# Kernel optimization log

Measured on AMD Instinct MI355X. Metric: run time of the kernel, lower is better.

Reference implementation:

```python
import jax, jax.numpy as jnp
import numpy as np

K = 20          # neighbors, hardcoded in module
SLOPE = 0.2     # LeakyReLU negative slope
EPS = 1e-5      # BatchNorm eps (eval mode, running_mean=0, running_var=1)


def _knn_idx(x, k):
    # x: (B, N, C) -> (B, N, k) indices of k nearest neighbors (includes self)
    xx = jnp.sum(x * x, axis=-1)                      # (B, N)
    inner = jnp.einsum('bnc,bmc->bnm', x, x)          # (B, N, N)
    neg_sqdist = 2.0 * inner - xx[:, :, None] - xx[:, None, :]
    _, idx = jax.lax.top_k(neg_sqdist, k)
    return idx


def _graph_feature(x, k):
    # x: (B, N, C) -> edge features (B, N, k, 2C) = [x_j - x_i, x_i]
    idx = _knn_idx(x, k)
    feat = jax.vmap(lambda xt, ix: xt[ix])(x, idx)    # (B, N, k, C)
    xc = jnp.broadcast_to(x[:, :, None, :], feat.shape)
    return jnp.concatenate([feat - xc, xc], axis=-1)


def _bn_lrelu(h, g, b):
    # eval-mode BN (mean=0, var=1) + LeakyReLU(0.2)
    h = h * (g / jnp.sqrt(1.0 + EPS)) + b
    return jnp.where(h >= 0, h, SLOPE * h)


def _edge_conv(x, W, g, b):
    # EdgeConv block: graph feature -> 1x1 conv -> BN -> LeakyReLU -> max over k
    e = _graph_feature(x, K)                          # (B, N, k, 2C)
    h = jnp.einsum('bnkc,oc->bnko', e, W)
    h = _bn_lrelu(h, g, b)
    return jnp.max(h, axis=2)                         # (B, N, O)


def reference(x, W1, g1, b1, W2, g2, b2, W3, g3, b3, W4, g4, b4, W5, g5, b5, Wemb):
    # x: (B, N, 3) point cloud
    x1 = _edge_conv(x, W1, g1, b1)    # (B, N, 64)
    x2 = _edge_conv(x1, W2, g2, b2)   # (B, N, 64)
    x3 = _edge_conv(x2, W3, g3, b3)   # (B, N, 128)
    x4 = _edge_conv(x3, W4, g4, b4)   # (B, N, 256)
    h = jnp.concatenate([x1, x2, x3, x4], axis=-1)    # (B, N, 512)
    h = jnp.einsum('bnc,oc->bno', h, W5)              # conv5 (1x1)
    h = _bn_lrelu(h, g5, b5)
    h = jnp.max(h, axis=1)                            # global max pool -> (B, 512)
    feat = h[:, None, :]                              # (B, 1, 512)
    embedding = h @ Wemb.T                            # (B, 256)
    return (feat, embedding)


def setup_inputs() -> dict:
    key = jax.random.key(0)
    ks = jax.random.split(key, 18)
    B, N = 8, 2048
    num_features = 256

    def w(k, o, i):
        return jax.random.normal(k, (o, i), dtype=jnp.float32) * (1.0 / np.sqrt(i))

    return {
        'x':  jax.random.normal(ks[0], (B, N, 3), dtype=jnp.float32),
        'W1': w(ks[1], 64, 6),
        'g1': jnp.ones((64,), jnp.float32),  'b1': jnp.zeros((64,), jnp.float32),
        'W2': w(ks[2], 64, 128),
        'g2': jnp.ones((64,), jnp.float32),  'b2': jnp.zeros((64,), jnp.float32),
        'W3': w(ks[3], 128, 128),
        'g3': jnp.ones((128,), jnp.float32), 'b3': jnp.zeros((128,), jnp.float32),
        'W4': w(ks[4], 256, 256),
        'g4': jnp.ones((256,), jnp.float32), 'b4': jnp.zeros((256,), jnp.float32),
        'W5': w(ks[5], 512, 512),
        'g5': jnp.ones((512,), jnp.float32), 'b5': jnp.zeros((512,), jnp.float32),
        'Wemb': w(ks[6], num_features, 512),
    }
```

## Files before the change

### kernel.cpp

```cpp
#include <hip/hip_runtime.h>
#include <hip/hip_bf16.h>

#define BB 8
#define NN 2048
#define KK 20
#define BN (BB*NN)
#define RSQ 0.99999500003749969f

constexpr size_t OFF_XX  = 0;
constexpr size_t OFF_X1  = OFF_XX  + BN;
constexpr size_t OFF_X2  = OFF_X1  + (size_t)BN*64;
constexpr size_t OFF_X3  = OFF_X2  + (size_t)BN*64;
constexpr size_t OFF_X4  = OFF_X3  + (size_t)BN*128;
constexpr size_t OFF_SC  = OFF_X4  + (size_t)BN*256;
constexpr size_t OFF_ID  = OFF_SC  + (size_t)BN*160;
constexpr size_t OFF_W5T = OFF_ID  + (size_t)BN*20;
constexpr size_t OFF_MX  = OFF_W5T + 512*512;
constexpr size_t OFF_MN  = OFF_MX  + BB*512;
constexpr size_t OFF_WT2 = OFF_MN  + BB*512;
constexpr size_t OFF_WT3 = OFF_WT2 + 8192;
constexpr size_t OFF_WT4 = OFF_WT3 + 16384;
constexpr size_t WS_END  = OFF_WT4 + 65536;
constexpr size_t OFF_BIG = WS_END;
constexpr size_t OFF_XCAT = OFF_BIG + (size_t)16*1024*1024;
constexpr size_t WS_BIG_END = OFF_BIG + (size_t)BB*NN*NN;
static_assert(OFF_ID - OFF_X3 >= (size_t)4096*2048, "fallback dual dist fits");
static_assert(OFF_XCAT + (size_t)BN*768 <= WS_BIG_END, "xcat h/m/l fits in dist region");

typedef unsigned short u16;
typedef __attribute__((ext_vector_type(8))) short short8;
typedef __attribute__((ext_vector_type(8))) unsigned short ushort8;
typedef __attribute__((ext_vector_type(4))) float f32x4;

constexpr size_t WTS_2H = 0,      WTS_2M = 8192,   WTS_2L = 16384;
constexpr size_t WTS_3H = 24576,  WTS_3M = 40960,  WTS_3L = 57344;
constexpr size_t WTS_4H = 73728,  WTS_4M = 139264, WTS_4L = 204800;

__device__ inline unsigned encf(float f){ unsigned u=__float_as_uint(f); return (u&0x80000000u)? ~u : (u|0x80000000u); }
__device__ inline float decf(unsigned e){ unsigned u=(e&0x80000000u)? (e&0x7fffffffu) : ~e; return __uint_as_float(u); }
__device__ inline float lrelu(float h){ return h>=0.f ? h : 0.2f*h; }
__device__ inline u16 bf16rne(float x){
  unsigned u = __float_as_uint(x);
  return (u16)((u + 0x7FFFu + ((u>>16)&1u)) >> 16);
}
__device__ inline float bf16f(u16 h){ return __uint_as_float((unsigned)h<<16); }
__device__ inline void bf16split3(float v, u16& h, u16& m, u16& l){
  h = bf16rne(v);  float r1 = v  - bf16f(h);
  m = bf16rne(r1); float r2 = r1 - bf16f(m);
  l = bf16rne(r2);
}

__device__ inline float readlane_f(float v, int sl){
  return __int_as_float(__builtin_amdgcn_readlane(__float_as_int(v), sl));
}

#define INSERT_CAND(cv, ci) { \
  unsigned long long mge = __ballot((lv > cv) || (lv == cv && li < ci)); \
  int pos = __popcll(mge); \
  float upv = __shfl_up(lv, 1); \
  int   upi = __shfl_up(li, 1); \
  bool shift = (lane > pos) && (lane < KK); \
  lv = (lane == pos) ? cv : (shift ? upv : lv); \
  li = (lane == pos) ? ci : (shift ? upi : li); \
  theta = readlane_f(lv, KK-1); }

#define BITONIC64_DESC(v, vi) { \
  _Pragma("unroll") \
  for(int k=2; k<=64; k<<=1){ \
    _Pragma("unroll") \
    for(int j=k>>1; j>=1; j>>=1){ \
      float ov = __shfl_xor(v, j); \
      int   oi = __shfl_xor(vi, j); \
      int partner = lane ^ j; \
      bool keepFirst = (((lane & k) == 0)) == (lane < partner); \
      bool before = (v > ov) || (v == ov && vi < oi); \
      if(keepFirst != before){ v = ov; vi = oi; } \
    } \
  } }


__global__ void prep_k(const float* W5, const float* W2, const float* W3, const float* W4,
                       float* W5T, float* WT2, float* WT3, float* WT4,
                       u16* w5h, u16* w5m, u16* w5l, u16* wts,
                       unsigned* mx, unsigned* mn, int big){
  int i = blockIdx.x*256 + threadIdx.x;
  if(!big){ int o = i>>9, c = i&511; W5T[c*512+o] = W5[i]; }
  {
    int rg = i>>13, kt = (i>>9)&15, l = (i>>3)&63, j = i&7;
    int o = rg*16 + (l&15);
    int c = kt*32 + ((l>>4)<<3) + j;
    u16 h,m,lo; bf16split3(W5[(size_t)o*512 + c], h, m, lo);
    w5h[i]=h; w5m[i]=m; w5l[i]=lo; }
  if(i < 65536){ int c = i>>9, o = i&511;
    WT4[i] = (o<256) ? W4[(size_t)o*256 + c] : W4[(size_t)(o-256)*256 + 128 + c]; }
  if(i < 16384){ int c = i>>8, o = i&255;
    WT3[i] = (o<128) ? W3[(size_t)o*128 + c] : W3[(size_t)(o-128)*128 + 64 + c]; }
  if(i <  8192){ int c = i>>7, o = i&127;
    WT2[i] = (o<64) ? W2[(size_t)o*128 + c] : W2[(size_t)(o-64)*128 + 64 + c]; }
  if(big){
    if(i < 65536){
      int rg=i>>11, kt=(i>>9)&3, l=(i>>3)&63, j=i&7;
      int o = rg*16 + (l&15);
      int c = kt*32 + ((l>>4)<<3) + j;
      float v = (o<256) ? W4[(size_t)o*256 + c] : W4[(size_t)(o-256)*256 + 128 + c];
      u16 h,m,lo; bf16split3(v,h,m,lo);
      wts[WTS_4H+i]=h; wts[WTS_4M+i]=m; wts[WTS_4L+i]=lo; }
  }
  if(i <  4096){ mx[i] = 0x007FFFFFu; mn[i] = 0xFF800000u; }
}

template<int C>
__launch_bounds__(256) __global__ void sqnorm_k(const float* X, float* xx){
  int i = blockIdx.x*256 + threadIdx.x;
  const float* r = X + (size_t)i*C;
  float s = 0.f;
  #pragma unroll
  for(int c=0;c<C;c++) s = fmaf(r[c], r[c], s);
  xx[i] = s;
}

template<int C>
__launch_bounds__(256) __global__ void split_k(const float* __restrict__ X,
    u16* __restrict__ xh, u16* __restrict__ xm, u16* __restrict__ xl){
  constexpr int KT = C/32;
  const size_t t = (size_t)blockIdx.x*256 + threadIdx.x;
  const int l = (int)(t & 63);
  const size_t tile = t >> 6;
  const int kt = (int)(tile & (KT-1));
  const size_t rgG = tile / KT;
  const size_t row = rgG*16 + (l & 15);
  const int k = kt*32 + ((l>>4)<<3);
  const float* p = X + row*C + k;
  float4 v0 = *(const float4*)p;
  float4 v1 = *(const float4*)(p+4);
  float vs[8] = {v0.x,v0.y,v0.z,v0.w,v1.x,v1.y,v1.z,v1.w};
  ushort8 H,M,L;
  #pragma unroll
  for(int j=0;j<8;j++){ u16 h,m,lo; bf16split3(vs[j],h,m,lo); H[j]=h; M[j]=m; L[j]=lo; }
  *(ushort8*)(xh + t*8) = H;
  *(ushort8*)(xm + t*8) = M;
  *(ushort8*)(xl + t*8) = L;
}

#define FMA_ROW(I) \
  acc[I][0]=fmaf(a,b0v,acc[I][0]); acc[I][1]=fmaf(a,b1v,acc[I][1]); \
  acc[I][2]=fmaf(a,b2v,acc[I][2]); acc[I][3]=fmaf(a,b3v,acc[I][3]); \
  acc[I][4]=fmaf(a,b4v,acc[I][4]); acc[I][5]=fmaf(a,b5v,acc[I][5]); \
  acc[I][6]=fmaf(a,b6v,acc[I][6]); acc[I][7]=fmaf(a,b7v,acc[I][7]);

template<int C>
__launch_bounds__(256) __global__ void gemm_dist_k(const float* __restrict__ X, const float* __restrict__ xx,
                                                   float* __restrict__ dist, int b0){
  constexpr int AST = 188;
  __shared__ __align__(16) float a_sh[16*AST];
  __shared__ __align__(16) float b_sh[16*AST];
  __shared__ float sxn[128], sxm[128];
  const int tid = threadIdx.x;
  const int b   = b0 + blockIdx.z;
  const int mtile = blockIdx.x*128;
  const int ntile = blockIdx.y*128;
  const int tn = tid & 15, tm = tid >> 4;
  const float* Xb  = X  + (size_t)b*NN*C;
  const float* xxb = xx + (size_t)b*NN;
  if(tid < 128) sxn[tid] = xxb[ntile + tid];
  else          sxm[tid-128] = xxb[mtile + tid-128];
  float acc[8][8];
  #pragma unroll
  for(int i=0;i<8;i++){
    #pragma unroll
    for(int j=0;j<8;j++) acc[i][j]=0.f;
  }
  for(int cc=0; cc<C; cc+=16){
    __syncthreads();
    #pragma unroll
    for(int s=0;s<2;s++){
      int ii = tid + 256*s; int r = ii>>2, q = ii&3;
      int pr = r + 4*(r>>3);
      float4 va = *(const float4*)&Xb[(size_t)(ntile + r)*C + cc + 4*q];
      a_sh[(4*q+0)*AST + pr]=va.x; a_sh[(4*q+1)*AST + pr]=va.y;
      a_sh[(4*q+2)*AST + pr]=va.z; a_sh[(4*q+3)*AST + pr]=va.w;
      float4 vb = *(const float4*)&Xb[(size_t)(mtile + r)*C + cc + 4*q];
      b_sh[(4*q+0)*AST + pr]=vb.x; b_sh[(4*q+1)*AST + pr]=vb.y;
      b_sh[(4*q+2)*AST + pr]=vb.z; b_sh[(4*q+3)*AST + pr]=vb.w;
    }
    __syncthreads();
    #pragma unroll
    for(int c=0;c<16;c++){
      float4 A0 = *(const float4*)&a_sh[c*AST + 12*tn];
      float4 A1 = *(const float4*)&a_sh[c*AST + 12*tn + 4];
      float4 B0 = *(const float4*)&b_sh[c*AST + 12*tm];
      float4 B1 = *(const float4*)&b_sh[c*AST + 12*tm + 4];
      float b0v=B0.x,b1v=B0.y,b2v=B0.z,b3v=B0.w,b4v=B1.x,b5v=B1.y,b6v=B1.z,b7v=B1.w;
      float a;
      a=A0.x; FMA_ROW(0)
      a=A0.y; FMA_ROW(1)
      a=A0.z; FMA_ROW(2)
      a=A0.w; FMA_ROW(3)
      a=A1.x; FMA_ROW(4)
      a=A1.y; FMA_ROW(5)
      a=A1.z; FMA_ROW(6)
      a=A1.w; FMA_ROW(7)
    }
  }
  float xnr[8], xmr[8];
  #pragma unroll
  for(int i=0;i<8;i++){ xnr[i]=sxn[tn*8+i]; xmr[i]=sxm[tm*8+i]; }
  const size_t rowb = (size_t)blockIdx.z*NN + ntile + tn*8;
  #pragma unroll
  for(int i=0;i<8;i++){
    float4 w0, w1;
    w0.x=(2.f*acc[i][0]-xnr[i])-xmr[0]; w0.y=(2.f*acc[i][1]-xnr[i])-xmr[1];
    w0.z=(2.f*acc[i][2]-xnr[i])-xmr[2]; w0.w=(2.f*acc[i][3]-xnr[i])-xmr[3];
    w1.x=(2.f*acc[i][4]-xnr[i])-xmr[4]; w1.y=(2.f*acc[i][5]-xnr[i])-xmr[5];
    w1.z=(2.f*acc[i][6]-xnr[i])-xmr[6]; w1.w=(2.f*acc[i][7]-xnr[i])-xmr[7];
    float* dp = dist + (rowb + i)*NN + mtile + tm*8;
    *(float4*)dp = w0;
    *(float4*)(dp+4) = w1;
  }
}

template<int C>
__launch_bounds__(256) __global__ void mfma_dist_k(const u16* __restrict__ xh, const u16* __restrict__ xm,
    const u16* __restrict__ xl, const float* __restrict__ xx, float* __restrict__ dist, int b0){
  constexpr int KT = C/32;
  const int tid = threadIdx.x;
  const int l  = tid & 63, wv = tid >> 6;
  const int lg = l >> 4, lr = l & 15;
  const int cz = blockIdx.z;
  const int b  = b0 + cz;
  const int qrow0 = blockIdx.y*128 + (wv>>1)*64;
  const int crow0 = blockIdx.x*128 + (wv&1)*64;
  const size_t brg = (size_t)b*(NN/16);
  f32x4 acc[4][4];
  #pragma unroll
  for(int m=0;m<4;m++){
    #pragma unroll
    for(int n=0;n<4;n++) acc[m][n] = (f32x4){0.f,0.f,0.f,0.f};
  }
  const size_t abase = (brg + (qrow0>>4))*KT*512 + (size_t)l*8;
  const size_t bbase = (brg + (crow0>>4))*KT*512 + (size_t)l*8;
  for(int kt=0; kt<KT; kt++){
    short8 Ah[4], Am[4], Al[4], Bh[4], Bm[4], Bl[4];
    #pragma unroll
    for(int m=0;m<4;m++){
      size_t o = abase + (size_t)(m*KT + kt)*512;
      Ah[m] = *(const short8*)(xh + o);
      Am[m] = *(const short8*)(xm + o);
      Al[m] = *(const short8*)(xl + o);
    }
    #pragma unroll
    for(int n=0;n<4;n++){
      size_t o = bbase + (size_t)(n*KT + kt)*512;
      Bh[n] = *(const short8*)(xh + o);
      Bm[n] = *(const short8*)(xm + o);
      Bl[n] = *(const short8*)(xl + o);
    }
    #pragma unroll
    for(int m=0;m<4;m++){
      #pragma unroll
      for(int n=0;n<4;n++){
        acc[m][n] = __builtin_amdgcn_mfma_f32_16x16x32_bf16(Ah[m], Bh[n], acc[m][n], 0, 0, 0);
        acc[m][n] = __builtin_amdgcn_mfma_f32_16x16x32_bf16(Ah[m], Bm[n], acc[m][n], 0, 0, 0);
        acc[m][n] = __builtin_amdgcn_mfma_f32_16x16x32_bf16(Am[m], Bh[n], acc[m][n], 0, 0, 0);
        acc[m][n] = __builtin_amdgcn_mfma_f32_16x16x32_bf16(Ah[m], Bl[n], acc[m][n], 0, 0, 0);
        acc[m][n] = __builtin_amdgcn_mfma_f32_16x16x32_bf16(Al[m], Bh[n], acc[m][n], 0, 0, 0);
        acc[m][n] = __builtin_amdgcn_mfma_f32_16x16x32_bf16(Am[m], Bm[n], acc[m][n], 0, 0, 0);
      }
    }
  }
  const float* xxb = xx + (size_t)b*NN;
  float xxc[4];
  #pragma unroll
  for(int n=0;n<4;n++) xxc[n] = xxb[crow0 + n*16 + lr];
  #pragma unroll
  for(int m=0;m<4;m++){
    #pragma unroll
    for(int r=0;r<4;r++){
      int qr = qrow0 + m*16 + 4*lg + r;
      float xq = xxb[qr];
      float* dp = dist + ((size_t)cz*NN + qr)*NN + crow0;
      #pragma unroll
      for(int n=0;n<4;n++) dp[n*16 + lr] = (2.f*acc[m][n][r] - xq) - xxc[n];
    }
  }
}

__launch_bounds__(256) __global__ void sel_k(const float* __restrict__ dist, int* __restrict__ id,
                                             int b0, int nrows){
  const int w = (blockIdx.x*256 + threadIdx.x) >> 6;
  const int lane = threadIdx.x & 63;
  if(w >= nrows) return;
  const float* dr = dist + (size_t)w*NN;
  float4 c0 = *(const float4*)&dr[4*lane];
  float cd0[4] = {c0.x, c0.y, c0.z, c0.w};
  int jbest = 0; float v = cd0[0];
  #pragma unroll
  for(int j=1;j<4;j++){ if(cd0[j] > v){ v = cd0[j]; jbest = j; } }
  int vi = 4*lane + jbest;
  BITONIC64_DESC(v, vi)
  float lv = (lane < KK) ? v : -INFINITY;
  int   li = (lane < KK) ? vi : 0;
  float theta = readlane_f(lv, KK-1);
  #pragma unroll
  for(int j=0;j<4;j++){
    float cand = (j == jbest) ? -INFINITY : cd0[j];
    unsigned long long bal = __ballot(cand > theta);
    while(bal){
      int bpos = __ffsll((unsigned long long)bal) - 1;
      bal &= bal - 1;
      float cv = readlane_f(cand, bpos);
      if(cv > theta){
        int ci = 4*bpos + j;
        INSERT_CAND(cv, ci)
      }
    }
  }
  for(int ms=256; ms<NN; ms+=256){
    float4 c4 = *(const float4*)&dr[ms + 4*lane];
    #pragma unroll
    for(int j=0;j<4;j++){
      float cand = (j==0)?c4.x:(j==1)?c4.y:(j==2)?c4.z:c4.w;
      unsigned long long bal = __ballot(cand > theta);
      while(bal){
        int bpos = __ffsll((unsigned long long)bal) - 1;
        bal &= bal - 1;
        float cv = readlane_f(cand, bpos);
        if(cv > theta){
          int ci = ms + 4*bpos + j;
          INSERT_CAND(cv, ci)
        }
      }
    }
  }
  if(lane < KK) id[((size_t)b0*NN + w)*KK + lane] = li;
}

__launch_bounds__(256) __global__ void sel3_k(const float* __restrict__ X, int* __restrict__ id){
  const int gw = (blockIdx.x*256 + threadIdx.x) >> 6;
  const int lane = threadIdx.x & 63;
  const int b = gw >> 11, n = gw & 2047;
  const float* Xb  = X + (size_t)b*NN*3;
  const float x0v = Xb[n*3], x1v = Xb[n*3+1], x2v = Xb[n*3+2];
  float xxn = 0.f;
  xxn = fmaf(x0v, x0v, xxn); xxn = fmaf(x1v, x1v, xxn); xxn = fmaf(x2v, x2v, xxn);
  float lv, theta; int li;
  {
    const float* p = Xb + (size_t)(4*lane)*3;
    float4 va = *(const float4*)p;
    float4 vb = *(const float4*)(p+4);
    float4 vc = *(const float4*)(p+8);
    float cx[4] = {va.x, va.w, vb.z, vc.y};
    float cy[4] = {va.y, vb.x, vb.w, vc.z};
    float cz[4] = {va.z, vb.y, vc.x, vc.w};
    float cd[4];
    #pragma unroll
    for(int j=0;j<4;j++){
      float s = 0.f;
      s = fmaf(x0v, cx[j], s); s = fmaf(x1v, cy[j], s); s = fmaf(x2v, cz[j], s);
      float xxm = 0.f;
      xxm = fmaf(cx[j], cx[j], xxm); xxm = fmaf(cy[j], cy[j], xxm); xxm = fmaf(cz[j], cz[j], xxm);
      cd[j] = (2.f*s - xxn) - xxm;
    }
    int jbest = 0; float v = cd[0];
    #pragma unroll
    for(int j=1;j<4;j++){ if(cd[j] > v){ v = cd[j]; jbest = j; } }
    int vi = 4*lane + jbest;
    BITONIC64_DESC(v, vi)
    lv = (lane < KK) ? v : -INFINITY;
    li = (lane < KK) ? vi : 0;
    theta = readlane_f(lv, KK-1);
    #pragma unroll
    for(int j=0;j<4;j++){
      float cand = (j == jbest) ? -INFINITY : cd[j];
      unsigned long long bal = __ballot(cand > theta);
      while(bal){
        int bpos = __ffsll((unsigned long long)bal) - 1;
        bal &= bal - 1;
        float cv = readlane_f(cand, bpos);
        if(cv > theta){
          int ci = 4*bpos + j;
          INSERT_CAND(cv, ci)
        }
      }
    }
  }
  for(int ms=256; ms<NN; ms+=256){
    const float* p = Xb + (size_t)(ms + 4*lane)*3;
    float4 va = *(const float4*)p;
    float4 vb = *(const float4*)(p+4);
    float4 vc = *(const float4*)(p+8);
    float cx[4] = {va.x, va.w, vb.z, vc.y};
    float cy[4] = {va.y, vb.x, vb.w, vc.z};
    float cz[4] = {va.z, vb.y, vc.x, vc.w};
    float cd[4];
    #pragma unroll
    for(int j=0;j<4;j++){
      float s = 0.f;
      s = fmaf(x0v, cx[j], s); s = fmaf(x1v, cy[j], s); s = fmaf(x2v, cz[j], s);
      float xxm = 0.f;
      xxm = fmaf(cx[j], cx[j], xxm); xxm = fmaf(cy[j], cy[j], xxm); xxm = fmaf(cz[j], cz[j], xxm);
      cd[j] = (2.f*s - xxn) - xxm;
    }
    #pragma unroll
    for(int j=0;j<4;j++){
      float cand = cd[j];
      unsigned long long bal = __ballot(cand > theta);
      while(bal){
        int bpos = __ffsll((unsigned long long)bal) - 1;
        bal &= bal - 1;
        float cv = readlane_f(cand, bpos);
        if(cv > theta){
          int ci = ms + 4*bpos + j;
          INSERT_CAND(cv, ci)
        }
      }
    }
  }
  if(lane < KK) id[(size_t)gw*KK + lane] = li;
}

__launch_bounds__(256) __global__ void qp3_k(const float* X, const float* W, float* qp){
  const int t   = blockIdx.x*256 + threadIdx.x;
  const int row = t >> 3;
  const int c0  = (t & 7) * 8;
  float xn[3];
  #pragma unroll
  for(int c=0;c<3;c++) xn[c] = X[(size_t)row*3 + c];
  for(int oi=c0; oi<c0+8; oi++){
    const float* w = W + (size_t)oi*6;
    float aq=0.f, ap=0.f;
    #pragma unroll
    for(int c=0;c<3;c++){ aq = fmaf(xn[c], w[c], aq); ap = fmaf(xn[c], w[3+c], ap); }
    qp[(size_t)row*128 + oi]      = aq;
    qp[(size_t)row*128 + 64 + oi] = ap;
  }
}

template<int CIN, int W2C>
__launch_bounds__(256) __global__ void qp_gemm_k(const float* __restrict__ X, const float* __restrict__ WT,
                                                 float* __restrict__ qp){
  constexpr int ASTA = 92;
  constexpr int ASTB = 188;
  __shared__ __align__(16) float a_sh[16*ASTA];
  __shared__ __align__(16) float b_sh[16*ASTB];
  const int tid = threadIdx.x;
  const int otile = blockIdx.x*128;
  const int rtile = blockIdx.y*64;
  const int tn = tid & 15, tm = tid >> 4;
  const int aoff = 4*tn + 4*(tn>>1);
  float acc[4][8];
  #pragma unroll
  for(int i=0;i<4;i++){
    #pragma unroll
    for(int j=0;j<8;j++) acc[i][j]=0.f;
  }
  for(int cc=0; cc<CIN; cc+=16){
    __syncthreads();
    { int r = tid>>2, q = tid&3;
      int pr = r + 4*(r>>3);
      float4 va = *(const float4*)&X[(size_t)(rtile + r)*CIN + cc + 4*q];
      a_sh[(4*q+0)*ASTA + pr]=va.x; a_sh[(4*q+1)*ASTA + pr]=va.y;
      a_sh[(4*q+2)*ASTA + pr]=va.z; a_sh[(4*q+3)*ASTA + pr]=va.w; }
    #pragma unroll
    for(int s=0;s<2;s++){
      int ii = tid + 256*s;
      int cl = ii>>5, o4 = ii&31;
      float4 vb = *(const float4*)&WT[(size_t)(cc+cl)*W2C + otile + 4*o4];
      *(float4*)&b_sh[cl*ASTB + 4*o4 + 4*(o4>>1)] = vb;
    }
    __syncthreads();
    #pragma unroll
    for(int c=0;c<16;c++){
      float4 A0 = *(const float4*)&a_sh[c*ASTA + aoff];
      float4 B0 = *(const float4*)&b_sh[c*ASTB + 12*tm];
      float4 B1 = *(const float4*)&b_sh[c*ASTB + 12*tm + 4];
      float b0v=B0.x,b1v=B0.y,b2v=B0.z,b3v=B0.w,b4v=B1.x,b5v=B1.y,b6v=B1.z,b7v=B1.w;
      float a;
      a=A0.x; FMA_ROW(0)
      a=A0.y; FMA_ROW(1)
      a=A0.z; FMA_ROW(2)
      a=A0.w; FMA_ROW(3)
    }
  }
  #pragma unroll
  for(int i=0;i<4;i++){
    float* dp = qp + (size_t)(rtile + tn*4 + i)*W2C + otile + tm*8;
    *(float4*)dp     = make_float4(acc[i][0],acc[i][1],acc[i][2],acc[i][3]);
    *(float4*)(dp+4) = make_float4(acc[i][4],acc[i][5],acc[i][6],acc[i][7]);
  }
}

__launch_bounds__(256) __global__ void qp_mfma4_k(const u16* __restrict__ xh, const u16* __restrict__ xm,
    const u16* __restrict__ xl,
    const u16* __restrict__ wh, const u16* __restrict__ wm, const u16* __restrict__ wl,
    float* __restrict__ qp){
  constexpr int KT = 4;
  const int tid = threadIdx.x;
  const int l  = tid & 63, wv = tid >> 6;
  const int lg = l >> 4, lr = l & 15;
  const int row0 = blockIdx.x*128 + (wv>>1)*64;
  const int col0 = blockIdx.y*128 + (wv&1)*64;
  f32x4 acc[4][4];
  #pragma unroll
  for(int m=0;m<4;m++){
    #pragma unroll
    for(int n=0;n<4;n++) acc[m][n] = (f32x4){0.f,0.f,0.f,0.f};
  }
  const size_t abase = (size_t)(row0>>4)*KT*512 + (size_t)l*8;
  const size_t bbase = (size_t)(col0>>4)*KT*512 + (size_t)l*8;
  for(int kt=0; kt<KT; kt++){
    short8 Ah[4], Am[4], Al[4], Bh[4], Bm[4], Bl[4];
    #pragma unroll
    for(int m=0;m<4;m++){
      size_t o = abase + (size_t)(m*KT + kt)*512;
      Ah[m] = *(const short8*)(xh + o);
      Am[m] = *(const short8*)(xm + o);
      Al[m] = *(const short8*)(xl + o);
    }
    #pragma unroll
    for(int n=0;n<4;n++){
      size_t o = bbase + (size_t)(n*KT + kt)*512;
      Bh[n] = *(const short8*)(wh + o);
      Bm[n] = *(const short8*)(wm + o);
      Bl[n] = *(const short8*)(wl + o);
    }
    #pragma unroll
    for(int m=0;m<4;m++){
      #pragma unroll
      for(int n=0;n<4;n++){
        acc[m][n] = __builtin_amdgcn_mfma_f32_16x16x32_bf16(Ah[m], Bh[n], acc[m][n], 0, 0, 0);
        acc[m][n] = __builtin_amdgcn_mfma_f32_16x16x32_bf16(Ah[m], Bm[n], acc[m][n], 0, 0, 0);
        acc[m][n] = __builtin_amdgcn_mfma_f32_16x16x32_bf16(Am[m], Bh[n], acc[m][n], 0, 0, 0);
        acc[m][n] = __builtin_amdgcn_mfma_f32_16x16x32_bf16(Ah[m], Bl[n], acc[m][n], 0, 0, 0);
        acc[m][n] = __builtin_amdgcn_mfma_f32_16x16x32_bf16(Al[m], Bh[n], acc[m][n], 0, 0, 0);
        acc[m][n] = __builtin_amdgcn_mfma_f32_16x16x32_bf16(Am[m], Bm[n], acc[m][n], 0, 0, 0);
      }
    }
  }
  #pragma unroll
  for(int m=0;m<4;m++){
    #pragma unroll
    for(int r=0;r<4;r++){
      int row = row0 + m*16 + 4*lg + r;
      float* dp = qp + (size_t)row*512 + col0;
      #pragma unroll
      for(int n=0;n<4;n++) dp[n*16 + lr] = acc[m][n][r];
    }
  }
}

template<int COUT>
__launch_bounds__(256) __global__ void gather_qp_k(const float* __restrict__ qp, const int* __restrict__ idx,
    const float* g, const float* bb, float* out){
  const int t  = blockIdx.x*256 + threadIdx.x;
  const int o  = t % COUT;
  const int bn = t / COUT;
  const int b  = bn >> 11;
  const int* id = idx + (size_t)bn*KK;
  float qv = qp[(size_t)bn*(2*COUT) + o];
  float pv = qp[(size_t)bn*(2*COUT) + COUT + o];
  float base = pv - qv;
  float mx = -INFINITY, mn = INFINITY;
  #pragma unroll
  for(int k=0;k<KK;k++){
    int ik = id[k];
    float v = qp[((size_t)((b<<11) + ik))*(2*COUT) + o];
    mx = fmaxf(mx, v); mn = fminf(mn, v);
  }
  float a  = g[o] * RSQ;
  float bo = bb[o];
  out[(size_t)bn*COUT + o] = lrelu((a >= 0.f ? a*(mx+base) : a*(mn+base)) + bo);
}

template<int CIN, int COUT>
__launch_bounds__(256) __global__ void qp64T_k(const float* __restrict__ X, const float* __restrict__ WT,
                                               int cb, float* __restrict__ q, float* __restrict__ bs){
  const int t   = blockIdx.x*256 + threadIdx.x;
  const int row = t >> 3;
  const int o0  = cb + (t & 7) * 8;
  float xn[CIN];
  #pragma unroll
  for(int c=0;c<CIN;c+=4){ float4 v = *(const float4*)(X + (size_t)row*CIN + c);
    xn[c]=v.x; xn[c+1]=v.y; xn[c+2]=v.z; xn[c+3]=v.w; }
  float aq[8], ap[8];
  #pragma unroll
  for(int j=0;j<8;j++){ aq[j]=0.f; ap[j]=0.f; }
  #pragma unroll 4
  for(int c=0;c<CIN;c++){
    float xc = xn[c];
    float4 wa0 = *(const float4*)&WT[(size_t)c*(2*COUT) + o0];
    float4 wa1 = *(const float4*)&WT[(size_t)c*(2*COUT) + o0 + 4];
    float4 wb0 = *(const float4*)&WT[(size_t)c*(2*COUT) + COUT + o0];
    float4 wb1 = *(const float4*)&WT[(size_t)c*(2*COUT) + COUT + o0 + 4];
    aq[0]=fmaf(xc,wa0.x,aq[0]); aq[1]=fmaf(xc,wa0.y,aq[1]); aq[2]=fmaf(xc,wa0.z,aq[2]); aq[3]=fmaf(xc,wa0.w,aq[3]);
    aq[4]=fmaf(xc,wa1.x,aq[4]); aq[5]=fmaf(xc,wa1.y,aq[5]); aq[6]=fmaf(xc,wa1.z,aq[6]); aq[7]=fmaf(xc,wa1.w,aq[7]);
    ap[0]=fmaf(xc,wb0.x,ap[0]); ap[1]=fmaf(xc,wb0.y,ap[1]); ap[2]=fmaf(xc,wb0.z,ap[2]); ap[3]=fmaf(xc,wb0.w,ap[3]);
    ap[4]=fmaf(xc,wb1.x,ap[4]); ap[5]=fmaf(xc,wb1.y,ap[5]); ap[6]=fmaf(xc,wb1.z,ap[6]); ap[7]=fmaf(xc,wb1.w,ap[7]);
  }
  float* qpp = q  + (size_t)row*64 + (o0-cb);
  float* bpp = bs + (size_t)row*64 + (o0-cb);
  *(float4*)qpp     = make_float4(aq[0],aq[1],aq[2],aq[3]);
  *(float4*)(qpp+4) = make_float4(aq[4],aq[5],aq[6],aq[7]);
  *(float4*)bpp     = make_float4(ap[0]-aq[0],ap[1]-aq[1],ap[2]-aq[2],ap[3]-aq[3]);
  *(float4*)(bpp+4) = make_float4(ap[4]-aq[4],ap[5]-aq[5],ap[6]-aq[6],ap[7]-aq[7]);
}

template<int CFULL>
__launch_bounds__(256) __global__ void gather_chunk_k(const float* q, const float* bs, const int* idx,
    const float* g, const float* bb, int cb, float* out){
  const int t  = blockIdx.x*256 + threadIdx.x;
  const int o  = t & 63;
  const int bn = t >> 6;
  const int b  = bn >> 11;
  const int* id = idx + (size_t)bn*KK;
  float base = bs[t];
  float mx = -INFINITY, mn = INFINITY;
  #pragma unroll
  for(int k=0;k<KK;k++){
    int ik = id[k];
    float v = q[((size_t)((b<<11) + ik))*64 + o];
    mx = fmaxf(mx, v); mn = fminf(mn, v);
  }
  float a  = g[cb+o] * RSQ;
  float bo = bb[cb+o];
  out[(size_t)bn*CFULL + cb + o] = lrelu((a >= 0.f ? a*(mx+base) : a*(mn+base)) + bo);
}

__launch_bounds__(256) __global__ void w5gemm_k(const float* __restrict__ x1, const float* __restrict__ x2,
    const float* __restrict__ x3, const float* __restrict__ x4,
// ... 21 lines not shown
    else if(cc<128){ src=x2; stride=64;  coff=cc-64; }
    else if(cc<256){ src=x3; stride=128; coff=cc-128; }
    else           { src=x4; stride=256; coff=cc-256; }
    __syncthreads();
    { int r = tid>>2, q = tid&3;
      int pr = r + 4*(r>>3);
      float4 va = *(const float4*)&src[(row0 + r)*stride + coff + 4*q];
      a_sh[(4*q+0)*ASTA + pr]=va.x; a_sh[(4*q+1)*ASTA + pr]=va.y;
      a_sh[(4*q+2)*ASTA + pr]=va.z; a_sh[(4*q+3)*ASTA + pr]=va.w; }
    #pragma unroll
    for(int s=0;s<2;s++){
      int ii = tid + 256*s;
      int cl = ii>>5, o4 = ii&31;
      float4 vb = *(const float4*)&W5T[(size_t)(cc+cl)*512 + otile + 4*o4];
      *(float4*)&b_sh[cl*ASTB + 4*o4 + 4*(o4>>1)] = vb;
    }
    __syncthreads();
    #pragma unroll
    for(int c=0;c<16;c++){
      float4 A0 = *(const float4*)&a_sh[c*ASTA + aoff];
      float4 B0 = *(const float4*)&b_sh[c*ASTB + 12*tm];
      float4 B1 = *(const float4*)&b_sh[c*ASTB + 12*tm + 4];
      float b0v=B0.x,b1v=B0.y,b2v=B0.z,b3v=B0.w,b4v=B1.x,b5v=B1.y,b6v=B1.z,b7v=B1.w;
      float a;
      a=A0.x; FMA_ROW(0)
      a=A0.y; FMA_ROW(1)
      a=A0.z; FMA_ROW(2)
      a=A0.w; FMA_ROW(3)
    }
  }
  #pragma unroll
  for(int j=0;j<8;j++){
    float M=-INFINITY, m=INFINITY;
    #pragma unroll
    for(int i=0;i<4;i++){ M=fmaxf(M,acc[i][j]); m=fminf(m,acc[i][j]); }
    #pragma unroll
    for(int d=1; d<16; d<<=1){
      M = fmaxf(M, __shfl_xor(M, d));
      m = fminf(m, __shfl_xor(m, d));
    }
    if(tn == 0){
      int o = otile + tm*8 + j;
      atomicMax(&mxe[b*512+o], encf(M));
      atomicMin(&mne[b*512+o], encf(m));
    }
  }
}

__launch_bounds__(256) __global__ void cvt_k(const float* __restrict__ x1, const float* __restrict__ x2,
    const float* __restrict__ x3, const float* __restrict__ x4,
    u16* __restrict__ xh, u16* __restrict__ xm, u16* __restrict__ xl){
  const size_t t = (size_t)blockIdx.x*256 + threadIdx.x;
  const int l = (int)(t & 63);
  const size_t tile = t >> 6;
  const int kt = (int)(tile & 15);
  const size_t rgG = tile >> 4;
  const size_t row = rgG*16 + (l & 15);
  const int col = kt*32 + ((l>>4)<<3);
  const float* src; int stride, coff;
  if(col<64)      { src=x1; stride=64;  coff=col; }
  else if(col<128){ src=x2; stride=64;  coff=col-64; }
  else if(col<256){ src=x3; stride=128; coff=col-128; }
  else            { src=x4; stride=256; coff=col-256; }
  const float* p = src + row*stride + coff;
  float4 v0 = *(const float4*)p;
  float4 v1 = *(const float4*)(p+4);
  float vs[8] = {v0.x,v0.y,v0.z,v0.w,v1.x,v1.y,v1.z,v1.w};
  ushort8 H, M, L;
  #pragma unroll
  for(int j=0;j<8;j++){ u16 h,m,lo; bf16split3(vs[j],h,m,lo); H[j]=h; M[j]=m; L[j]=lo; }
  *(ushort8*)(xh + t*8) = H;
  *(ushort8*)(xm + t*8) = M;
  *(ushort8*)(xl + t*8) = L;
}

__launch_bounds__(256) __global__ void w5mfma_k(const u16* __restrict__ xh, const u16* __restrict__ xm,
    const u16* __restrict__ xl,
    const u16* __restrict__ wh, const u16* __restrict__ wm, const u16* __restrict__ wl,
    unsigned* mxe, unsigned* mne){
  const int tid = threadIdx.x;
  const int l  = tid & 63, wv = tid >> 6;
  const int lg = l >> 4, lr = l & 15;
  const int row0 = blockIdx.x*128 + (wv>>1)*64;
  const int col0 = blockIdx.y*128 + (wv&1)*64;
  const int b = blockIdx.x >> 4;
  f32x4 acc[4][4];
  #pragma unroll
  for(int m=0;m<4;m++){
    #pragma unroll
    for(int n=0;n<4;n++) acc[m][n] = (f32x4){0.f,0.f,0.f,0.f};
  }
  const size_t abase = (size_t)(row0>>4)*16*512 + (size_t)l*8;
  const size_t bbase = (size_t)(col0>>4)*16*512 + (size_t)l*8;
  for(int kt=0; kt<16; kt++){
    short8 Ah[4], Am[4], Al[4], Bh[4], Bm[4], Bl[4];
    #pragma unroll
    for(int m=0;m<4;m++){
      size_t o = abase + (size_t)(m*16 + kt)*512;
      Ah[m] = *(const short8*)(xh + o);
      Am[m] = *(const short8*)(xm + o);
      Al[m] = *(const short8*)(xl + o);
    }
    #pragma unroll
    for(int n=0;n<4;n++){
      size_t o = bbase + (size_t)(n*16 + kt)*512;
      Bh[n] = *(const short8*)(wh + o);
      Bm[n] = *(const short8*)(wm + o);
      Bl[n] = *(const short8*)(wl + o);
    }
    #pragma unroll
    for(int m=0;m<4;m++){
      #pragma unroll
      for(int n=0;n<4;n++){
        acc[m][n] = __builtin_amdgcn_mfma_f32_16x16x32_bf16(Ah[m], Bh[n], acc[m][n], 0, 0, 0);
        acc[m][n] = __builtin_amdgcn_mfma_f32_16x16x32_bf16(Ah[m], Bm[n], acc[m][n], 0, 0, 0);
        acc[m][n] = __builtin_amdgcn_mfma_f32_16x16x32_bf16(Am[m], Bh[n], acc[m][n], 0, 0, 0);
        acc[m][n] = __builtin_amdgcn_mfma_f32_16x16x32_bf16(Ah[m], Bl[n], acc[m][n], 0, 0, 0);
        acc[m][n] = __builtin_amdgcn_mfma_f32_16x16x32_bf16(Al[m], Bh[n], acc[m][n], 0, 0, 0);
        acc[m][n] = __builtin_amdgcn_mfma_f32_16x16x32_bf16(Am[m], Bm[n], acc[m][n], 0, 0, 0);
      }
    }
  }
  #pragma unroll
  for(int n=0;n<4;n++){
    float M = -INFINITY, mnv = INFINITY;
    #pragma unroll
    for(int m=0;m<4;m++){
      #pragma unroll
      for(int r=0;r<4;r++){ float v = acc[m][n][r]; M = fmaxf(M, v); mnv = fminf(mnv, v); }
    }
    M   = fmaxf(M,   __shfl_xor(M, 16));   M   = fmaxf(M,   __shfl_xor(M, 32));
    mnv = fminf(mnv, __shfl_xor(mnv, 16)); mnv = fminf(mnv, __shfl_xor(mnv, 32));
    if(lg == 0){
      int o = col0 + n*16 + lr;
      atomicMax(&mxe[b*512+o], encf(M));
      atomicMin(&mne[b*512+o], encf(mnv));
    }
  }
}

__launch_bounds__(256) __global__ void final_k(const unsigned* mxe, const unsigned* mne,
    const float* g5, const float* b5, const float* Wemb, float* out){
  const int b = blockIdx.x, t = threadIdx.x;
  __shared__ float h[512];
  for(int o=t; o<512; o+=256){
    float mx = decf(mxe[b*512+o]);
    float mn = decf(mne[b*512+o]);
    float a  = g5[o] * RSQ;
    float bo = b5[o];
    float hv = lrelu((a >= 0.f ? a*mx : a*mn) + bo);
    h[o] = hv;
    out[b*512+o] = hv;
  }
  __syncthreads();
  const float* wr = Wemb + (size_t)t*512;
  float s = 0.f;
  for(int o=0;o<512;o+=4){
    float4 w4 = *(const float4*)(wr+o);
    s = fmaf(h[o],w4.x, fmaf(h[o+1],w4.y, fmaf(h[o+2],w4.z, fmaf(h[o+3],w4.w, s))));
  }
  out[4096 + b*256 + t] = s;
}

extern "C" void kernel_launch(void* const* d_in, const int* in_sizes, int n_in,
                              void* d_out, int out_size, void* d_ws, size_t ws_size,
                              hipStream_t stream) {
  if (ws_size < WS_END * sizeof(float)) return;
  const bool big = ws_size >= WS_BIG_END * sizeof(float);

  const float* x0   = (const float*)d_in[0];
  const float* W1   = (const float*)d_in[1];
  const float* g1   = (const float*)d_in[2];
  const float* b1   = (const float*)d_in[3];
  const float* W2   = (const float*)d_in[4];
  const float* g2   = (const float*)d_in[5];
  const float* b2   = (const float*)d_in[6];
  const float* W3   = (const float*)d_in[7];
  const float* g3   = (const float*)d_in[8];
  const float* b3   = (const float*)d_in[9];
  const float* W4   = (const float*)d_in[10];
  const float* g4   = (const float*)d_in[11];
  const float* b4   = (const float*)d_in[12];
  const float* W5   = (const float*)d_in[13];
  const float* g5   = (const float*)d_in[14];
  const float* b5   = (const float*)d_in[15];
  const float* Wemb = (const float*)d_in[16];

  float* ws = (float*)d_ws;
  float* xx = ws + OFF_XX;
  float* x1 = ws + OFF_X1;  float* x2 = ws + OFF_X2;
  float* x3 = ws + OFF_X3;  float* x4 = ws + OFF_X4;
  float* qpS = ws + OFF_SC;
  float* bsS = ws + OFF_SC + (size_t)BN*64;
  int*   id = (int*)(ws + OFF_ID);
  float* W5Tf = ws + OFF_W5T;
  unsigned* mxe = (unsigned*)(ws + OFF_MX);
  unsigned* mne = (unsigned*)(ws + OFF_MN);
  float* WT2 = ws + OFF_WT2;
  float* WT3 = ws + OFF_WT3;
  float* WT4 = ws + OFF_WT4;
  float* distD = ws + OFF_X3;
  float* distS = ws + OFF_X4;
  float* distB = ws + OFF_BIG;
  u16* w5h = (u16*)(ws + OFF_SC + (size_t)BN*128);
  u16* w5m = w5h + 512*512;
  u16* w5l = w5m + 512*512;
  u16* wts = (u16*)W5Tf;
  float* out = (float*)d_out;

  prep_k<<<1024,256,0,stream>>>(W5, W2, W3, W4, W5Tf, WT2, WT3, WT4,
                                w5h, w5m, w5l, wts, mxe, mne, big ? 1 : 0);

  sel3_k<<<BN*64/256,256,0,stream>>>(x0, id);
  qp3_k<<<BN*8/256,256,0,stream>>>(x0, W1, qpS);
  gather_qp_k<64><<<BN*64/256,256,0,stream>>>(qpS, id, g1, b1, x1);

  if(big){
    float* qpB = distB;
    u16* sh = (u16*)x4;
    { u16* sm = sh + (size_t)BN*64; u16* sl = sm + (size_t)BN*64;
      sqnorm_k<64><<<BN/256,256,0,stream>>>(x1, xx);
      split_k<64><<<BN*64/8/256,256,0,stream>>>(x1, sh, sm, sl);
      for(int c0=0;c0<BB;c0+=4){
        mfma_dist_k<64><<<dim3(16,16,4),256,0,stream>>>(sh, sm, sl, xx, distB, c0);
        sel_k<<<(4*NN)/4,256,0,stream>>>(distB, id, c0, 4*NN);
      }
      qp_gemm_k<64,128><<<dim3(1,BN/64),256,0,stream>>>(x1, WT2, qpB);
      gather_qp_k<64><<<BN*64/256,256,0,stream>>>(qpB, id, g2, b2, x2); }
    { u16* sm = sh + (size_t)BN*64; u16* sl = sm + (size_t)BN*64;
      sqnorm_k<64><<<BN/256,256,0,stream>>>(x2, xx);
      split_k<64><<<BN*64/8/256,256,0,stream>>>(x2, sh, sm, sl);
      for(int c0=0;c0<BB;c0+=4){
        mfma_dist_k<64><<<dim3(16,16,4),256,0,stream>>>(sh, sm, sl, xx, distB, c0);
        sel_k<<<(4*NN)/4,256,0,stream>>>(distB, id, c0, 4*NN);
      }
      qp_gemm_k<64,256><<<dim3(2,BN/64),256,0,stream>>>(x2, WT3, qpB);
      gather_qp_k<128><<<BN*128/256,256,0,stream>>>(qpB, id, g3, b3, x3); }
    { u16* sm = sh + (size_t)BN*128; u16* sl = sm + (size_t)BN*128;
      sqnorm_k<128><<<BN/256,256,0,stream>>>(x3, xx);
      split_k<128><<<BN*128/8/256,256,0,stream>>>(x3, sh, sm, sl);
      for(int c0=0;c0<BB;c0+=4){
        mfma_dist_k<128><<<dim3(16,16,4),256,0,stream>>>(sh, sm, sl, xx, distB, c0);
        sel_k<<<(4*NN)/4,256,0,stream>>>(distB, id, c0, 4*NN);
      }
      qp_mfma4_k<<<dim3(BN/128,4),256,0,stream>>>(sh, sm, sl,
          wts+WTS_4H, wts+WTS_4M, wts+WTS_4L, qpB);
      gather_qp_k<256><<<BN*256/256,256,0,stream>>>(qpB, id, g4, b4, x4); }
    u16* xh = (u16*)(ws + OFF_XCAT);
    u16* xm = xh + (size_t)BN*512;
    u16* xl = xm + (size_t)BN*512;
    cvt_k<<<BN*512/8/256,256,0,stream>>>(x1, x2, x3, x4, xh, xm, xl);
    w5mfma_k<<<dim3(128,4),256,0,stream>>>(xh, xm, xl, w5h, w5m, w5l, mxe, mne);
  } else {
    sqnorm_k<64><<<BN/256,256,0,stream>>>(x1, xx);
    for(int r=0;r<4;r++){
      gemm_dist_k<64><<<dim3(16,16,2),256,0,stream>>>(x1, xx, distD, 2*r);
      sel_k<<<(2*NN)/4,256,0,stream>>>(distD, id, 2*r, 2*NN);
    }
    qp64T_k<64,64><<<BN*8/256,256,0,stream>>>(x1, WT2, 0, qpS, bsS);
    gather_chunk_k<64><<<BN*64/256,256,0,stream>>>(qpS, bsS, id, g2, b2, 0, x2);

    sqnorm_k<64><<<BN/256,256,0,stream>>>(x2, xx);
    for(int r=0;r<4;r++){
      gemm_dist_k<64><<<dim3(16,16,2),256,0,stream>>>(x2, xx, distD, 2*r);
      sel_k<<<(2*NN)/4,256,0,stream>>>(distD, id, 2*r, 2*NN);
    }
    for(int cb=0; cb<128; cb+=64){
      qp64T_k<64,128><<<BN*8/256,256,0,stream>>>(x2, WT3, cb, qpS, bsS);
      gather_chunk_k<128><<<BN*64/256,256,0,stream>>>(qpS, bsS, id, g3, b3, cb, x3);
    }

    sqnorm_k<128><<<BN/256,256,0,stream>>>(x3, xx);
    for(int r=0;r<8;r++){
      gemm_dist_k<128><<<dim3(16,16,1),256,0,stream>>>(x3, xx, distS, r);
      sel_k<<<NN/4,256,0,stream>>>(distS, id, r, NN);
    }
    for(int cb=0; cb<256; cb+=64){
      qp64T_k<128,256><<<BN*8/256,256,0,stream>>>(x3, WT4, cb, qpS, bsS);
      gather_chunk_k<256><<<BN*64/256,256,0,stream>>>(qpS, bsS, id, g4, b4, cb, x4);
    }
    w5gemm_k<<<dim3(4,32,8),256,0,stream>>>(x1, x2, x3, x4, W5Tf, mxe, mne);
  }

  final_k<<<BB,256,0,stream>>>(mxe, mne, g5, b5, Wemb, out);
}
```

Measured before the change: 610.3 us.

## Shrink MFMA wave tiles to 64x32 and move layer-2/3 projections to split-bf16 MFMA

Halves the column tile of the MFMA distance, projection and conv5 kernels (4x2 accumulators per wave instead of 4x4) and doubles the grid, which lowers register pressure and raises the number of blocks. It also replaces the fp32 shared-memory SIMT GEMM used for the layer-2 and layer-3 point projections with a templated split-bf16 MFMA kernel. That kernel reuses the already-split activations and new pre-split W2/W3 weights prepared in the prep kernel. In exchange, the A operands are reloaded by twice as many blocks, and the projections now rely on the three-way bf16 split accuracy instead of fp32 FMA.

```diff
diff --git a/kernel.cpp b/kernel.cpp
--- a/kernel.cpp
+++ b/kernel.cpp
@@ -77,6 +77,14 @@
       if(keepFirst != before){ v = ov; vi = oi; } \
     } \
   } }
+
+#define MFMA6(ACC, AH, AM, AL, BH, BM, BL) { \
+  ACC = __builtin_amdgcn_mfma_f32_16x16x32_bf16(AH, BH, ACC, 0, 0, 0); \
+  ACC = __builtin_amdgcn_mfma_f32_16x16x32_bf16(AH, BM, ACC, 0, 0, 0); \
+  ACC = __builtin_amdgcn_mfma_f32_16x16x32_bf16(AM, BH, ACC, 0, 0, 0); \
+  ACC = __builtin_amdgcn_mfma_f32_16x16x32_bf16(AH, BL, ACC, 0, 0, 0); \
+  ACC = __builtin_amdgcn_mfma_f32_16x16x32_bf16(AL, BH, ACC, 0, 0, 0); \
+  ACC = __builtin_amdgcn_mfma_f32_16x16x32_bf16(AM, BM, ACC, 0, 0, 0); }
 
 
 __global__ void prep_k(const float* W5, const float* W2, const float* W3, const float* W4,
@@ -105,6 +113,20 @@
       float v = (o<256) ? W4[(size_t)o*256 + c] : W4[(size_t)(o-256)*256 + 128 + c];
       u16 h,m,lo; bf16split3(v,h,m,lo);
       wts[WTS_4H+i]=h; wts[WTS_4M+i]=m; wts[WTS_4L+i]=lo; }
+    if(i < 16384){
+      int rg=i>>10, kt=(i>>9)&1, l=(i>>3)&63, j=i&7;
+      int o = rg*16 + (l&15);
+      int c = kt*32 + ((l>>4)<<3) + j;
+      float v = (o<128) ? W3[(size_t)o*128 + c] : W3[(size_t)(o-128)*128 + 64 + c];
+      u16 h,m,lo; bf16split3(v,h,m,lo);
+      wts[WTS_3H+i]=h; wts[WTS_3M+i]=m; wts[WTS_3L+i]=lo; }
+    if(i < 8192){
+      int rg=i>>10, kt=(i>>9)&1, l=(i>>3)&63, j=i&7;
+      int o = rg*16 + (l&15);
+      int c = kt*32 + ((l>>4)<<3) + j;
+      float v = (o<64) ? W2[(size_t)o*128 + c] : W2[(size_t)(o-64)*128 + 64 + c];
+      u16 h,m,lo; bf16split3(v,h,m,lo);
+      wts[WTS_2H+i]=h; wts[WTS_2M+i]=m; wts[WTS_2L+i]=lo; }
   }
   if(i <  4096){ mx[i] = 0x007FFFFFu; mn[i] = 0xFF800000u; }
 }
@@ -229,18 +251,18 @@
   const int cz = blockIdx.z;
   const int b  = b0 + cz;
   const int qrow0 = blockIdx.y*128 + (wv>>1)*64;
-  const int crow0 = blockIdx.x*128 + (wv&1)*64;
+  const int crow0 = blockIdx.x*64 + (wv&1)*32;
   const size_t brg = (size_t)b*(NN/16);
-  f32x4 acc[4][4];
+  f32x4 acc[4][2];
   #pragma unroll
   for(int m=0;m<4;m++){
     #pragma unroll
-    for(int n=0;n<4;n++) acc[m][n] = (f32x4){0.f,0.f,0.f,0.f};
+    for(int n=0;n<2;n++) acc[m][n] = (f32x4){0.f,0.f,0.f,0.f};
   }
   const size_t abase = (brg + (qrow0>>4))*KT*512 + (size_t)l*8;
   const size_t bbase = (brg + (crow0>>4))*KT*512 + (size_t)l*8;
   for(int kt=0; kt<KT; kt++){
-    short8 Ah[4], Am[4], Al[4], Bh[4], Bm[4], Bl[4];
+    short8 Ah[4], Am[4], Al[4], Bh[2], Bm[2], Bl[2];
     #pragma unroll
     for(int m=0;m<4;m++){
       size_t o = abase + (size_t)(m*KT + kt)*512;
@@ -249,7 +271,7 @@
       Al[m] = *(const short8*)(xl + o);
     }
     #pragma unroll
-    for(int n=0;n<4;n++){
+    for(int n=0;n<2;n++){
       size_t o = bbase + (size_t)(n*KT + kt)*512;
       Bh[n] = *(const short8*)(xh + o);
       Bm[n] = *(const short8*)(xm + o);
@@ -258,20 +280,15 @@
     #pragma unroll
     for(int m=0;m<4;m++){
       #pragma unroll
-      for(int n=0;n<4;n++){
-        acc[m][n] = __builtin_amdgcn_mfma_f32_16x16x32_bf16(Ah[m], Bh[n], acc[m][n], 0, 0, 0);
-        acc[m][n] = __builtin_amdgcn_mfma_f32_16x16x32_bf16(Ah[m], Bm[n], acc[m][n], 0, 0, 0);
-        acc[m][n] = __builtin_amdgcn_mfma_f32_16x16x32_bf16(Am[m], Bh[n], acc[m][n], 0, 0, 0);
-        acc[m][n] = __builtin_amdgcn_mfma_f32_16x16x32_bf16(Ah[m], Bl[n], acc[m][n], 0, 0, 0);
-        acc[m][n] = __builtin_amdgcn_mfma_f32_16x16x32_bf16(Al[m], Bh[n], acc[m][n], 0, 0, 0);
-        acc[m][n] = __builtin_amdgcn_mfma_f32_16x16x32_bf16(Am[m], Bm[n], acc[m][n], 0, 0, 0);
+      for(int n=0;n<2;n++){
+        MFMA6(acc[m][n], Ah[m], Am[m], Al[m], Bh[n], Bm[n], Bl[n])
       }
     }
   }
   const float* xxb = xx + (size_t)b*NN;
-  float xxc[4];
-  #pragma unroll
-  for(int n=0;n<4;n++) xxc[n] = xxb[crow0 + n*16 + lr];
+  float xxc[2];
+  #pragma unroll
+  for(int n=0;n<2;n++) xxc[n] = xxb[crow0 + n*16 + lr];
   #pragma unroll
   for(int m=0;m<4;m++){
     #pragma unroll
@@ -280,7 +297,7 @@
       float xq = xxb[qr];
       float* dp = dist + ((size_t)cz*NN + qr)*NN + crow0;
       #pragma unroll
-      for(int n=0;n<4;n++) dp[n*16 + lr] = (2.f*acc[m][n][r] - xq) - xxc[n];
+      for(int n=0;n<2;n++) dp[n*16 + lr] = (2.f*acc[m][n][r] - xq) - xxc[n];
     }
   }
 }
@@ -436,80 +453,26 @@
   }
 }
 
-template<int CIN, int W2C>
-__launch_bounds__(256) __global__ void qp_gemm_k(const float* __restrict__ X, const float* __restrict__ WT,
-                                                 float* __restrict__ qp){
-  constexpr int ASTA = 92;
-  constexpr int ASTB = 188;
-  __shared__ __align__(16) float a_sh[16*ASTA];
-  __shared__ __align__(16) float b_sh[16*ASTB];
-  const int tid = threadIdx.x;
-  const int otile = blockIdx.x*128;
-  const int rtile = blockIdx.y*64;
-  const int tn = tid & 15, tm = tid >> 4;
-  const int aoff = 4*tn + 4*(tn>>1);
-  float acc[4][8];
-  #pragma unroll
-  for(int i=0;i<4;i++){
-    #pragma unroll
-    for(int j=0;j<8;j++) acc[i][j]=0.f;
-  }
-  for(int cc=0; cc<CIN; cc+=16){
-    __syncthreads();
-    { int r = tid>>2, q = tid&3;
-      int pr = r + 4*(r>>3);
-      float4 va = *(const float4*)&X[(size_t)(rtile + r)*CIN + cc + 4*q];
-      a_sh[(4*q+0)*ASTA + pr]=va.x; a_sh[(4*q+1)*ASTA + pr]=va.y;
-      a_sh[(4*q+2)*ASTA + pr]=va.z; a_sh[(4*q+3)*ASTA + pr]=va.w; }
-    #pragma unroll
-    for(int s=0;s<2;s++){
-      int ii = tid + 256*s;
-      int cl = ii>>5, o4 = ii&31;
-      float4 vb = *(const float4*)&WT[(size_t)(cc+cl)*W2C + otile + 4*o4];
-      *(float4*)&b_sh[cl*ASTB + 4*o4 + 4*(o4>>1)] = vb;
-    }
-    __syncthreads();
-    #pragma unroll
-    for(int c=0;c<16;c++){
-      float4 A0 = *(const float4*)&a_sh[c*ASTA + aoff];
-      float4 B0 = *(const float4*)&b_sh[c*ASTB + 12*tm];
-      float4 B1 = *(const float4*)&b_sh[c*ASTB + 12*tm + 4];
-      float b0v=B0.x,b1v=B0.y,b2v=B0.z,b3v=B0.w,b4v=B1.x,b5v=B1.y,b6v=B1.z,b7v=B1.w;
-      float a;
-      a=A0.x; FMA_ROW(0)
-      a=A0.y; FMA_ROW(1)
-      a=A0.z; FMA_ROW(2)
-      a=A0.w; FMA_ROW(3)
-    }
-  }
-  #pragma unroll
-  for(int i=0;i<4;i++){
-    float* dp = qp + (size_t)(rtile + tn*4 + i)*W2C + otile + tm*8;
-    *(float4*)dp     = make_float4(acc[i][0],acc[i][1],acc[i][2],acc[i][3]);
-    *(float4*)(dp+4) = make_float4(acc[i][4],acc[i][5],acc[i][6],acc[i][7]);
-  }
-}
-
-__launch_bounds__(256) __global__ void qp_mfma4_k(const u16* __restrict__ xh, const u16* __restrict__ xm,
+template<int KT, int W2C>
+__launch_bounds__(256) __global__ void qp_mfma_k(const u16* __restrict__ xh, const u16* __restrict__ xm,
     const u16* __restrict__ xl,
     const u16* __restrict__ wh, const u16* __restrict__ wm, const u16* __restrict__ wl,
     float* __restrict__ qp){
-  constexpr int KT = 4;
   const int tid = threadIdx.x;
   const int l  = tid & 63, wv = tid >> 6;
   const int lg = l >> 4, lr = l & 15;
   const int row0 = blockIdx.x*128 + (wv>>1)*64;
-  const int col0 = blockIdx.y*128 + (wv&1)*64;
-  f32x4 acc[4][4];
+  const int col0 = blockIdx.y*64 + (wv&1)*32;
+  f32x4 acc[4][2];
   #pragma unroll
   for(int m=0;m<4;m++){
     #pragma unroll
-    for(int n=0;n<4;n++) acc[m][n] = (f32x4){0.f,0.f,0.f,0.f};
+    for(int n=0;n<2;n++) acc[m][n] = (f32x4){0.f,0.f,0.f,0.f};
   }
   const size_t abase = (size_t)(row0>>4)*KT*512 + (size_t)l*8;
   const size_t bbase = (size_t)(col0>>4)*KT*512 + (size_t)l*8;
   for(int kt=0; kt<KT; kt++){
-    short8 Ah[4], Am[4], Al[4], Bh[4], Bm[4], Bl[4];
+    short8 Ah[4], Am[4], Al[4], Bh[2], Bm[2], Bl[2];
     #pragma unroll
     for(int m=0;m<4;m++){
       size_t o = abase + (size_t)(m*KT + kt)*512;
@@ -518,7 +481,7 @@
       Al[m] = *(const short8*)(xl + o);
     }
     #pragma unroll
-    for(int n=0;n<4;n++){
+    for(int n=0;n<2;n++){
       size_t o = bbase + (size_t)(n*KT + kt)*512;
       Bh[n] = *(const short8*)(wh + o);
       Bm[n] = *(const short8*)(wm + o);
@@ -527,13 +490,8 @@
     #pragma unroll
     for(int m=0;m<4;m++){
       #pragma unroll
-      for(int n=0;n<4;n++){
-        acc[m][n] = __builtin_amdgcn_mfma_f32_16x16x32_bf16(Ah[m], Bh[n], acc[m][n], 0, 0, 0);
-        acc[m][n] = __builtin_amdgcn_mfma_f32_16x16x32_bf16(Ah[m], Bm[n], acc[m][n], 0, 0, 0);
-        acc[m][n] = __builtin_amdgcn_mfma_f32_16x16x32_bf16(Am[m], Bh[n], acc[m][n], 0, 0, 0);
-        acc[m][n] = __builtin_amdgcn_mfma_f32_16x16x32_bf16(Ah[m], Bl[n], acc[m][n], 0, 0, 0);
-        acc[m][n] = __builtin_amdgcn_mfma_f32_16x16x32_bf16(Al[m], Bh[n], acc[m][n], 0, 0, 0);
-        acc[m][n] = __builtin_amdgcn_mfma_f32_16x16x32_bf16(Am[m], Bm[n], acc[m][n], 0, 0, 0);
+      for(int n=0;n<2;n++){
+        MFMA6(acc[m][n], Ah[m], Am[m], Al[m], Bh[n], Bm[n], Bl[n])
       }
     }
   }
@@ -542,9 +500,9 @@
     #pragma unroll
     for(int r=0;r<4;r++){
       int row = row0 + m*16 + 4*lg + r;
-      float* dp = qp + (size_t)row*512 + col0;
+      float* dp = qp + (size_t)row*W2C + col0;
       #pragma unroll
-      for(int n=0;n<4;n++) dp[n*16 + lr] = acc[m][n][r];
+      for(int n=0;n<2;n++) dp[n*16 + lr] = acc[m][n][r];
     }
   }
 }
@@ -732,18 +690,18 @@
   const int l  = tid & 63, wv = tid >> 6;
   const int lg = l >> 4, lr = l & 15;
   const int row0 = blockIdx.x*128 + (wv>>1)*64;
-  const int col0 = blockIdx.y*128 + (wv&1)*64;
+  const int col0 = blockIdx.y*64 + (wv&1)*32;
   const int b = blockIdx.x >> 4;
-  f32x4 acc[4][4];
+  f32x4 acc[4][2];
   #pragma unroll
   for(int m=0;m<4;m++){
     #pragma unroll
-    for(int n=0;n<4;n++) acc[m][n] = (f32x4){0.f,0.f,0.f,0.f};
+    for(int n=0;n<2;n++) acc[m][n] = (f32x4){0.f,0.f,0.f,0.f};
   }
   const size_t abase = (size_t)(row0>>4)*16*512 + (size_t)l*8;
   const size_t bbase = (size_t)(col0>>4)*16*512 + (size_t)l*8;
   for(int kt=0; kt<16; kt++){
-    short8 Ah[4], Am[4], Al[4], Bh[4], Bm[4], Bl[4];
+    short8 Ah[4], Am[4], Al[4], Bh[2], Bm[2], Bl[2];
     #pragma unroll
     for(int m=0;m<4;m++){
       size_t o = abase + (size_t)(m*16 + kt)*512;
@@ -752,7 +710,7 @@
       Al[m] = *(const short8*)(xl + o);
     }
     #pragma unroll
-    for(int n=0;n<4;n++){
+    for(int n=0;n<2;n++){
       size_t o = bbase + (size_t)(n*16 + kt)*512;
       Bh[n] = *(const short8*)(wh + o);
       Bm[n] = *(const short8*)(wm + o);
@@ -761,18 +719,13 @@
     #pragma unroll
     for(int m=0;m<4;m++){
       #pragma unroll
-      for(int n=0;n<4;n++){
-        acc[m][n] = __builtin_amdgcn_mfma_f32_16x16x32_bf16(Ah[m], Bh[n], acc[m][n], 0, 0, 0);
-        acc[m][n] = __builtin_amdgcn_mfma_f32_16x16x32_bf16(Ah[m], Bm[n], acc[m][n], 0, 0, 0);
-        acc[m][n] = __builtin_amdgcn_mfma_f32_16x16x32_bf16(Am[m], Bh[n], acc[m][n], 0, 0, 0);
-        acc[m][n] = __builtin_amdgcn_mfma_f32_16x16x32_bf16(Ah[m], Bl[n], acc[m][n], 0, 0, 0);
-        acc[m][n] = __builtin_amdgcn_mfma_f32_16x16x32_bf16(Al[m], Bh[n], acc[m][n], 0, 0, 0);
-        acc[m][n] = __builtin_amdgcn_mfma_f32_16x16x32_bf16(Am[m], Bm[n], acc[m][n], 0, 0, 0);
-      }
-    }
-  }
-  #pragma unroll
-  for(int n=0;n<4;n++){
+      for(int n=0;n<2;n++){
+        MFMA6(acc[m][n], Ah[m], Am[m], Al[m], Bh[n], Bm[n], Bl[n])
+      }
+    }
+  }
+  #pragma unroll
+  for(int n=0;n<2;n++){
     float M = -INFINITY, mnv = INFINITY;
     #pragma unroll
     for(int m=0;m<4;m++){
@@ -872,35 +825,37 @@
       sqnorm_k<64><<<BN/256,256,0,stream>>>(x1, xx);
       split_k<64><<<BN*64/8/256,256,0,stream>>>(x1, sh, sm, sl);
       for(int c0=0;c0<BB;c0+=4){
-        mfma_dist_k<64><<<dim3(16,16,4),256,0,stream>>>(sh, sm, sl, xx, distB, c0);
+        mfma_dist_k<64><<<dim3(32,16,4),256,0,stream>>>(sh, sm, sl, xx, distB, c0);
         sel_k<<<(4*NN)/4,256,0,stream>>>(distB, id, c0, 4*NN);
       }
-      qp_gemm_k<64,128><<<dim3(1,BN/64),256,0,stream>>>(x1, WT2, qpB);
+      qp_mfma_k<2,128><<<dim3(BN/128,2),256,0,stream>>>(sh, sm, sl,
+          wts+WTS_2H, wts+WTS_2M, wts+WTS_2L, qpB);
       gather_qp_k<64><<<BN*64/256,256,0,stream>>>(qpB, id, g2, b2, x2); }
     { u16* sm = sh + (size_t)BN*64; u16* sl = sm + (size_t)BN*64;
       sqnorm_k<64><<<BN/256,256,0,stream>>>(x2, xx);
       split_k<64><<<BN*64/8/256,256,0,stream>>>(x2, sh, sm, sl);
       for(int c0=0;c0<BB;c0+=4){
-        mfma_dist_k<64><<<dim3(16,16,4),256,0,stream>>>(sh, sm, sl, xx, distB, c0);
+        mfma_dist_k<64><<<dim3(32,16,4),256,0,stream>>>(sh, sm, sl, xx, distB, c0);
         sel_k<<<(4*NN)/4,256,0,stream>>>(distB, id, c0, 4*NN);
       }
-      qp_gemm_k<64,256><<<dim3(2,BN/64),256,0,stream>>>(x2, WT3, qpB);
+      qp_mfma_k<2,256><<<dim3(BN/128,4),256,0,stream>>>(sh, sm, sl,
+          wts+WTS_3H, wts+WTS_3M, wts+WTS_3L, qpB);
       gather_qp_k<128><<<BN*128/256,256,0,stream>>>(qpB, id, g3, b3, x3); }
     { u16* sm = sh + (size_t)BN*128; u16* sl = sm + (size_t)BN*128;
       sqnorm_k<128><<<BN/256,256,0,stream>>>(x3, xx);
       split_k<128><<<BN*128/8/256,256,0,stream>>>(x3, sh, sm, sl);
       for(int c0=0;c0<BB;c0+=4){
-        mfma_dist_k<128><<<dim3(16,16,4),256,0,stream>>>(sh, sm, sl, xx, distB, c0);
+        mfma_dist_k<128><<<dim3(32,16,4),256,0,stream>>>(sh, sm, sl, xx, distB, c0);
         sel_k<<<(4*NN)/4,256,0,stream>>>(distB, id, c0, 4*NN);
       }
-      qp_mfma4_k<<<dim3(BN/128,4),256,0,stream>>>(sh, sm, sl,
+      qp_mfma_k<4,512><<<dim3(BN/128,8),256,0,stream>>>(sh, sm, sl,
           wts+WTS_4H, wts+WTS_4M, wts+WTS_4L, qpB);
       gather_qp_k<256><<<BN*256/256,256,0,stream>>>(qpB, id, g4, b4, x4); }
     u16* xh = (u16*)(ws + OFF_XCAT);
     u16* xm = xh + (size_t)BN*512;
     u16* xl = xm + (size_t)BN*512;
     cvt_k<<<BN*512/8/256,256,0,stream>>>(x1, x2, x3, x4, xh, xm, xl);
-    w5mfma_k<<<dim3(128,4),256,0,stream>>>(xh, xm, xl, w5h, w5m, w5l, mxe, mne);
+    w5mfma_k<<<dim3(128,8),256,0,stream>>>(xh, xm, xl, w5h, w5m, w5l, mxe, mne);
   } else {
     sqnorm_k<64><<<BN/256,256,0,stream>>>(x1, xx);
     for(int r=0;r<4;r++){
```

New measurement: 603.4 us (median of 2 runs). Within noise of the previous version (-1.1%).
